# Kernel tuning notes

Measured on AMD Instinct MI355X. Metric: run time of the kernel, lower is better.

Reference implementation:

```python
import jax, jax.numpy as jnp
import numpy as np

N_NODES = 50000
N_EDGES = 800000
D = 64
N_GRAPHS = 512
N_LAYERS = 3
HID_FC = 64
N_CLASSES = 10


def setup_inputs() -> dict:
    key = jax.random.key(0)
    ks = jax.random.split(key, 12)
    s = 1.0 / np.sqrt(D)
    x = jax.random.normal(ks[0], (N_NODES, D), dtype=jnp.float32)
    edge_index = jax.random.randint(ks[1], (2, N_EDGES), 0, N_NODES, dtype=jnp.int32)
    batch = jnp.sort(jax.random.randint(ks[2], (N_NODES,), 0, N_GRAPHS, dtype=jnp.int32))
    convW1 = jax.random.normal(ks[3], (N_LAYERS, D, D), dtype=jnp.float32) * s
    convb1 = jax.random.normal(ks[4], (N_LAYERS, D), dtype=jnp.float32) * 0.01
    convW2 = jax.random.normal(ks[5], (N_LAYERS, D, D), dtype=jnp.float32) * s
    convb2 = jax.random.normal(ks[6], (N_LAYERS, D), dtype=jnp.float32) * 0.01
    fcW1 = jax.random.normal(ks[7], (D, HID_FC), dtype=jnp.float32) * s
    fcb1 = jax.random.normal(ks[8], (HID_FC,), dtype=jnp.float32) * 0.01
    fcW2 = jax.random.normal(ks[9], (HID_FC, N_CLASSES), dtype=jnp.float32) * (1.0 / np.sqrt(HID_FC))
    fcb2 = jax.random.normal(ks[10], (N_CLASSES,), dtype=jnp.float32) * 0.01
    return {"x": x, "convW1": convW1, "convb1": convb1, "convW2": convW2,
            "convb2": convb2, "fcW1": fcW1, "fcb1": fcb1, "fcW2": fcW2,
            "fcb2": fcb2, "edge_index": edge_index, "batch": batch}


def reference(x, convW1, convb1, convW2, convb2, fcW1, fcb1, fcW2, fcb2, edge_index, batch):
    src, dst = edge_index[0], edge_index[1]
    h = x
    for l in range(N_LAYERS):
        # GIN aggregation: (1 + eps) * x + sum_{j in N(i)} x_j, eps = 0
        agg = jax.ops.segment_sum(h[src], dst, num_segments=N_NODES)
        h = h + agg
        # per-layer MLP: Linear -> ReLU -> Linear
        h = jax.nn.relu(h @ convW1[l] + convb1[l])
        h = h @ convW2[l] + convb2[l]
    # global max pool over nodes of each graph
    g = jax.ops.segment_max(h, batch, num_segments=N_GRAPHS)
    # FC head: Linear(64) -> ReLU -> Linear(num_classes)
    g = jax.nn.relu(g @ fcW1 + fcb1)
    logits = g @ fcW2 + fcb2
    return jax.nn.log_softmax(logits, axis=1)
```

## Files before the change

### kernel.cpp

```cpp
#include <hip/hip_runtime.h>
#include <math.h>

#define N_NODES 50000
#define N_EDGES 800000
#define D 64
#define N_GRAPHS 512
#define N_CLASSES 10
#define NT 3125
#define NB32 1563
#define NPART 6250

#define SCAN_B 512
#define NB_SCAN ((N_NODES + SCAN_B - 1) / SCAN_B)

typedef __attribute__((ext_vector_type(8))) short bf16x8;
typedef __attribute__((ext_vector_type(4))) float f32x4;

#define MFMA16(a, b, c) __builtin_amdgcn_mfma_f32_16x16x32_bf16(a, b, c, 0, 0, 0)


__device__ __forceinline__ unsigned mapf(float f) {
  unsigned u = __float_as_uint(f);
  return (u & 0x80000000u) ? ~u : (u | 0x80000000u);
}
__device__ __forceinline__ float unmapf(unsigned u) {
  return __uint_as_float((u & 0x80000000u) ? (u & 0x7FFFFFFFu) : ~u);
}
__device__ __forceinline__ ushort bf16_rne(float f) {
  unsigned u = __float_as_uint(f);
  u += 0x7FFFu + ((u >> 16) & 1u);
  return (ushort)(u >> 16);
}
__device__ __forceinline__ float bf16_tof(ushort h) {
  return __uint_as_float(((unsigned)h) << 16);
}
__device__ __forceinline__ unsigned pack2(float a, float b) {
  return (unsigned)bf16_rne(a) | ((unsigned)bf16_rne(b) << 16);
}
__device__ __forceinline__ float2 unpack2(unsigned v) {
  return make_float2(__uint_as_float(v << 16), __uint_as_float(v & 0xFFFF0000u));
}


__global__ void wprep(const float* __restrict__ convW1, const float* __restrict__ convW2,
                      ushort* __restrict__ wf) {
  const int wi = blockIdx.x;
  const int layer = wi >> 1, which = wi & 1;
  const float* W = (which ? convW2 : convW1) + layer * 4096;
  const int t = threadIdx.x;
  const int f = t >> 6, lane = t & 63;
  const int ct = f >> 1, ks = f & 1;
  const int n = ct * 16 + (lane & 15);
  const int k0 = ks * 32 + ((lane >> 4) << 3);
  ushort hi[8], lo[8];
#pragma unroll
  for (int v = 0; v < 8; ++v) {
    float w = W[(k0 + v) * 64 + n];
    ushort h = bf16_rne(w);
    hi[v] = h;
    lo[v] = bf16_rne(w - bf16_tof(h));
  }
  ushort* base = wf + layer * 16384 + which * 8192;
  *(uint4*)(base + f * 512 + lane * 8) = *(uint4*)hi;
  *(uint4*)(base + 4096 + f * 512 + lane * 8) = *(uint4*)lo;
}


__global__ void hist_part(const int* __restrict__ dst, int* __restrict__ deg) {
  const int p = blockIdx.x & 7;
  const int lo = p * NPART, hi = lo + NPART;
  const int stride = (gridDim.x >> 3) * 256;
  for (int e = (blockIdx.x >> 3) * 256 + threadIdx.x; e < N_EDGES; e += stride) {
    int d = dst[e];
    if (d >= lo && d < hi) atomicAdd(&deg[d], 1);
  }
}

__global__ void scan_blocks(const int* __restrict__ deg, int* __restrict__ bsum) {
  __shared__ int sd[SCAN_B];
  int i = blockIdx.x * SCAN_B + threadIdx.x;
  sd[threadIdx.x] = (i < N_NODES) ? deg[i] : 0;
  __syncthreads();
  for (int off = SCAN_B / 2; off > 0; off >>= 1) {
    if (threadIdx.x < off) sd[threadIdx.x] += sd[threadIdx.x + off];
    __syncthreads();
  }
  if (threadIdx.x == 0) bsum[blockIdx.x] = sd[0];
}

__global__ void scan_mid(int* __restrict__ bsum) {
  __shared__ int s[256];
  int t = threadIdx.x;
  if (t < NB_SCAN) s[t] = bsum[t];
  __syncthreads();
  if (t == 0) {
    int run = 0;
    for (int i = 0; i < NB_SCAN; ++i) { int v = s[i]; s[i] = run; run += v; }
  }
  __syncthreads();
  if (t < NB_SCAN) bsum[t] = s[t];
}

__global__ void scan_final(const int* __restrict__ deg, const int* __restrict__ bsum,
                           int* __restrict__ rs, int* __restrict__ cur) {
  __shared__ int sd[SCAN_B];
  int i = blockIdx.x * SCAN_B + threadIdx.x;
  int v = (i < N_NODES) ? deg[i] : 0;
  sd[threadIdx.x] = v;
  __syncthreads();
  for (int off = 1; off < SCAN_B; off <<= 1) {
    int add = (threadIdx.x >= off) ? sd[threadIdx.x - off] : 0;
    __syncthreads();
    sd[threadIdx.x] += add;
    __syncthreads();
  }
  if (i < N_NODES) {
    int ex = bsum[blockIdx.x] + sd[threadIdx.x] - v;
    rs[i] = ex;
    cur[i] = ex;
  }
  if (i == 0) rs[N_NODES] = N_EDGES;
}

__global__ void fill_part(const int* __restrict__ src, const int* __restrict__ dst,
                          int* __restrict__ cur, int* __restrict__ csr) {
  const int p = blockIdx.x & 7;
  const int lo = p * NPART, hi = lo + NPART;
  const int stride = (gridDim.x >> 3) * 256;
  for (int e = (blockIdx.x >> 3) * 256 + threadIdx.x; e < N_EDGES; e += stride) {
    int d = dst[e];
    if (d >= lo && d < hi) {
      int pos = atomicAdd(&cur[d], 1);
      csr[pos] = src[e];
    }
  }
}


template <int FINAL, int F32IN>
__global__ __launch_bounds__(256, 4) void gin32(
    const void* __restrict__ hin_, unsigned* __restrict__ hout,
    const int* __restrict__ csr, const int* __restrict__ rs,
    const ushort* __restrict__ wfL,
    const float* __restrict__ b1, const float* __restrict__ b2,
    const int* __restrict__ batch, unsigned* __restrict__ gU) {
  __shared__ ushort Wl[16384];
  __shared__ ushort At[32][72];
  const int t = threadIdx.x;

  {
    const uint4* s = (const uint4*)wfL;
    uint4* d = (uint4*)Wl;
#pragma unroll
    for (int i = 0; i < 8; ++i) d[t + 256 * i] = s[t + 256 * i];
  }

  {
    const int qw = t >> 4, ql = t & 15;
    const float4* hf = (const float4*)hin_;
    const uint2* hb = (const uint2*)hin_;
#pragma unroll
    for (int i = 0; i < 2; ++i) {
      const int nl = qw + 16 * i;
      const int node = blockIdx.x * 32 + nl;
      float ax = 0.f, ay = 0.f, az = 0.f, aw = 0.f;
      if (node < N_NODES) {
        if (F32IN) {
          float4 v = hf[node * 16 + ql];
          ax = v.x; ay = v.y; az = v.z; aw = v.w;
        } else {
          uint2 u = hb[node * 16 + ql];
          float2 p0 = unpack2(u.x), p1 = unpack2(u.y);
          ax = p0.x; ay = p0.y; az = p1.x; aw = p1.y;
        }
        int e = rs[node];
        const int e1 = rs[node + 1];
        if (F32IN) {
          for (; e + 4 <= e1; e += 4) {
            int s0 = csr[e], s1 = csr[e + 1], s2 = csr[e + 2], s3 = csr[e + 3];
            float4 v0 = hf[s0 * 16 + ql];
            float4 v1 = hf[s1 * 16 + ql];
            float4 v2 = hf[s2 * 16 + ql];
            float4 v3 = hf[s3 * 16 + ql];
            ax += v0.x + v1.x; ay += v0.y + v1.y; az += v0.z + v1.z; aw += v0.w + v1.w;
            ax += v2.x + v3.x; ay += v2.y + v3.y; az += v2.z + v3.z; aw += v2.w + v3.w;
          }
          for (; e < e1; ++e) {
            float4 v = hf[csr[e] * 16 + ql];
            ax += v.x; ay += v.y; az += v.z; aw += v.w;
          }
        } else {
          for (; e + 4 <= e1; e += 4) {
            int s0 = csr[e], s1 = csr[e + 1], s2 = csr[e + 2], s3 = csr[e + 3];
            uint2 u0 = hb[s0 * 16 + ql];
            uint2 u1 = hb[s1 * 16 + ql];
            uint2 u2 = hb[s2 * 16 + ql];
            uint2 u3 = hb[s3 * 16 + ql];
            float2 q0, q1;
            q0 = unpack2(u0.x); q1 = unpack2(u0.y); ax += q0.x; ay += q0.y; az += q1.x; aw += q1.y;
            q0 = unpack2(u1.x); q1 = unpack2(u1.y); ax += q0.x; ay += q0.y; az += q1.x; aw += q1.y;
            q0 = unpack2(u2.x); q1 = unpack2(u2.y); ax += q0.x; ay += q0.y; az += q1.x; aw += q1.y;
            q0 = unpack2(u3.x); q1 = unpack2(u3.y); ax += q0.x; ay += q0.y; az += q1.x; aw += q1.y;
          }
          for (; e < e1; ++e) {
            uint2 u = hb[csr[e] * 16 + ql];
            float2 q0 = unpack2(u.x), q1 = unpack2(u.y);
            ax += q0.x; ay += q0.y; az += q1.x; aw += q1.y;
          }
        }
      }
      *(uint2*)&At[nl][4 * ql] = make_uint2(pack2(ax, ay), pack2(az, aw));
    }
  }
  __syncthreads();

  const int w = t >> 6, lane = t & 63;
  if (w >= 2) return;
  const int tile = blockIdx.x * 2 + w;
  if (tile >= NT) return;
  const int m = lane & 15, g = lane >> 4;
  ushort* tw = &At[w * 16][0];

  bf16x8 a0 = *(const bf16x8*)&At[w * 16 + m][g * 8];
  bf16x8 a1 = *(const bf16x8*)&At[w * 16 + m][32 + g * 8];
  const char* wb = (const char*)Wl + lane * 16;
#define LDW(off) (*(const bf16x8*)(wb + (off)))

  f32x4 c0 = {0.f, 0.f, 0.f, 0.f}, c1 = c0, c2 = c0, c3 = c0;
#define G1(ct, cc)                                      \
  cc = MFMA16(a0, LDW((2 * ct + 0) * 1024), cc);        \
  cc = MFMA16(a1, LDW((2 * ct + 1) * 1024), cc);        \
  cc = MFMA16(a0, LDW(8192 + (2 * ct + 0) * 1024), cc); \
  cc = MFMA16(a1, LDW(8192 + (2 * ct + 1) * 1024), cc);
  G1(0, c0) G1(1, c1) G1(2, c2) G1(3, c3)
#undef G1

  {
    float bv0 = b1[m], bv1 = b1[16 + m], bv2 = b1[32 + m], bv3 = b1[48 + m];
#define WRT(cc, ct, bv)                                                    \
    tw[(g * 4 + 0) * 72 + ct * 16 + m] = bf16_rne(fmaxf(cc[0] + bv, 0.f)); \
    tw[(g * 4 + 1) * 72 + ct * 16 + m] = bf16_rne(fmaxf(cc[1] + bv, 0.f)); \
    tw[(g * 4 + 2) * 72 + ct * 16 + m] = bf16_rne(fmaxf(cc[2] + bv, 0.f)); \
    tw[(g * 4 + 3) * 72 + ct * 16 + m] = bf16_rne(fmaxf(cc[3] + bv, 0.f));
    WRT(c0, 0, bv0) WRT(c1, 1, bv1) WRT(c2, 2, bv2) WRT(c3, 3, bv3)
#undef WRT
  }
  bf16x8 h0 = *(const bf16x8*)(tw + m * 72 + g * 8);
  bf16x8 h1 = *(const bf16x8*)(tw + m * 72 + 32 + g * 8);

  c0 = (f32x4){0.f, 0.f, 0.f, 0.f}; c1 = c0; c2 = c0; c3 = c0;
#define G2(ct, cc)                                       \
  cc = MFMA16(h0, LDW(16384 + (2 * ct + 0) * 1024), cc); \
  cc = MFMA16(h1, LDW(16384 + (2 * ct + 1) * 1024), cc); \
  cc = MFMA16(h0, LDW(24576 + (2 * ct + 0) * 1024), cc); \
  cc = MFMA16(h1, LDW(24576 + (2 * ct + 1) * 1024), cc);
  G2(0, c0) G2(1, c1) G2(2, c2) G2(3, c3)
#undef G2
#undef LDW

  const float bv20 = b2[m], bv21 = b2[16 + m], bv22 = b2[32 + m], bv23 = b2[48 + m];
  if (FINAL) {
    const int tb = tile * 16;
#define PM(cc, ct, bv, j)                                           \
    atomicMax(&gU[batch[tb + g * 4 + j] * 64 + ct * 16 + m], mapf(cc[j] + bv));
#define PM4(cc, ct, bv) PM(cc, ct, bv, 0) PM(cc, ct, bv, 1) PM(cc, ct, bv, 2) PM(cc, ct, bv, 3)
    PM4(c0, 0, bv20) PM4(c1, 1, bv21) PM4(c2, 2, bv22) PM4(c3, 3, bv23)
#undef PM4
#undef PM
  } else {
#define WRO(cc, ct, bv)                                        \
    tw[(g * 4 + 0) * 72 + ct * 16 + m] = bf16_rne(cc[0] + bv); \
    tw[(g * 4 + 1) * 72 + ct * 16 + m] = bf16_rne(cc[1] + bv); \
    tw[(g * 4 + 2) * 72 + ct * 16 + m] = bf16_rne(cc[2] + bv); \
    tw[(g * 4 + 3) * 72 + ct * 16 + m] = bf16_rne(cc[3] + bv);
    WRO(c0, 0, bv20) WRO(c1, 1, bv21) WRO(c2, 2, bv22) WRO(c3, 3, bv23)
#undef WRO
    const int r = lane >> 2, q = lane & 3;
    uint4 v0 = *(const uint4*)(tw + r * 72 + q * 16);
    uint4 v1 = *(const uint4*)(tw + r * 72 + q * 16 + 8);
    ushort* Ao = (ushort*)hout + (size_t)tile * 1024;
    *(uint4*)(Ao + lane * 16) = v0;
    *(uint4*)(Ao + lane * 16 + 8) = v1;
  }
}


__global__ void init_g(unsigned* __restrict__ gU) {
  int i = blockIdx.x * blockDim.x + threadIdx.x;
  if (i < N_GRAPHS * D) gU[i] = 0x007FFFFFu;
}

__global__ void head_kernel(const unsigned* __restrict__ gU,
                            const float* __restrict__ fcW1, const float* __restrict__ fcb1,
                            const float* __restrict__ fcW2, const float* __restrict__ fcb2,
                            float* __restrict__ out) {
  __shared__ float gbuf[64];
  __shared__ float hid[64];
  __shared__ float logit[N_CLASSES];
  __shared__ float red[2];
  const int gi = blockIdx.x;
  const int t = threadIdx.x;

  gbuf[t] = unmapf(gU[gi * D + t]);
  __syncthreads();

  float a = fcb1[t];
#pragma unroll
  for (int k = 0; k < 64; ++k) a = fmaf(gbuf[k], fcW1[k * 64 + t], a);
  hid[t] = fmaxf(a, 0.0f);
  __syncthreads();

  if (t < N_CLASSES) {
    float l = fcb2[t];
#pragma unroll
    for (int k = 0; k < 64; ++k) l = fmaf(hid[k], fcW2[k * N_CLASSES + t], l);
    logit[t] = l;
  }
  __syncthreads();

  if (t == 0) {
    float mx = logit[0];
    for (int i = 1; i < N_CLASSES; ++i) mx = fmaxf(mx, logit[i]);
    float s = 0.0f;
    for (int i = 0; i < N_CLASSES; ++i) s += expf(logit[i] - mx);
    red[0] = mx;
    red[1] = logf(s);
  }
  __syncthreads();

  if (t < N_CLASSES) out[gi * N_CLASSES + t] = logit[t] - red[0] - red[1];
}


extern "C" void kernel_launch(void* const* d_in, const int* in_sizes, int n_in,
                              void* d_out, int out_size, void* d_ws, size_t ws_size,
                              hipStream_t stream) {
  const float* x      = (const float*)d_in[0];
  const float* convW1 = (const float*)d_in[1];
  const float* convb1 = (const float*)d_in[2];
  const float* convW2 = (const float*)d_in[3];
  const float* convb2 = (const float*)d_in[4];
  const float* fcW1   = (const float*)d_in[5];
  const float* fcb1   = (const float*)d_in[6];
  const float* fcW2   = (const float*)d_in[7];
  const float* fcb2   = (const float*)d_in[8];
  const int*   edge   = (const int*)d_in[9];
  const int*   batch  = (const int*)d_in[10];
  float* out = (float*)d_out;

  const int* src = edge;
  const int* dst = edge + N_EDGES;

  unsigned* hbA = (unsigned*)d_ws;
  unsigned* hbB = hbA + (size_t)N_NODES * 32;
  unsigned* gU  = hbB + (size_t)N_NODES * 32;
  int* rs  = (int*)(gU + N_GRAPHS * D);
  int* csr = rs + N_NODES + 1;
  ushort* wf = (ushort*)(csr + N_EDGES);
  int* deg  = (int*)hbA;
  int* cur  = deg + N_NODES;
  int* bsum = cur + N_NODES;

  wprep<<<6, 512, 0, stream>>>(convW1, convW2, wf);
  init_g<<<(N_GRAPHS * D + 255) / 256, 256, 0, stream>>>(gU);

  hipMemsetAsync(deg, 0, N_NODES * sizeof(int), stream);
  hist_part<<<2048, 256, 0, stream>>>(dst, deg);
  scan_blocks<<<NB_SCAN, SCAN_B, 0, stream>>>(deg, bsum);
  scan_mid<<<1, 256, 0, stream>>>(bsum);
  scan_final<<<NB_SCAN, SCAN_B, 0, stream>>>(deg, bsum, rs, cur);
  fill_part<<<2048, 256, 0, stream>>>(src, dst, cur, csr);

  gin32<0, 1><<<NB32, 256, 0, stream>>>(x, hbA, csr, rs, wf,
                                        convb1, convb2, batch, gU);
  gin32<0, 0><<<NB32, 256, 0, stream>>>(hbA, hbB, csr, rs, wf + 16384,
                                        convb1 + 64, convb2 + 64, batch, gU);
  gin32<1, 0><<<NB32, 256, 0, stream>>>(hbB, nullptr, csr, rs, wf + 32768,
                                        convb1 + 128, convb2 + 128, batch, gU);

  head_kernel<<<N_GRAPHS, 64, 0, stream>>>(gU, fcW1, fcb1, fcW2, fcb2, out);
}
```

Before: 229.4 us.

## Fuse three GIN layer kernels into one persistent kernel with grid barriers

Replaces the three per-layer gin32 launches with a single persistent kernel of 1024 blocks that loops over node tiles and separates layers with a software grid barrier built on global atomics. The goal is to remove the launch gaps and tail drain between layers. In exchange, each block processes up to two tiles serially. The spin barrier depends on all 1024 blocks being co-resident, which the launch bounds (4 blocks per CU) should allow on 256 CUs.

```diff
diff --git a/kernel.cpp b/kernel.cpp
--- a/kernel.cpp
+++ b/kernel.cpp
@@ -9,6 +9,7 @@
 #define NT 3125
 #define NB32 1563
 #define NPART 6250
+#define MEGA_GRID 1024
 
 #define SCAN_B 512
 #define NB_SCAN ((N_NODES + SCAN_B - 1) / SCAN_B)
@@ -137,24 +138,42 @@
 }
 
 
-template <int FINAL, int F32IN>
-__global__ __launch_bounds__(256, 4) void gin32(
-    const void* __restrict__ hin_, unsigned* __restrict__ hout,
+__device__ __forceinline__ void stage_weights(const ushort* __restrict__ wfL,
+                                              ushort* Wl, int t) {
+  const uint4* s = (const uint4*)wfL;
+  uint4* d = (uint4*)Wl;
+#pragma unroll
+  for (int i = 0; i < 8; ++i) d[t + 256 * i] = s[t + 256 * i];
+}
+
+__device__ __forceinline__ void grid_barrier(unsigned* bar, int nb, int t) {
+  __threadfence();
+  __syncthreads();
+  if (t == 0) {
+    unsigned g = atomicAdd(&bar[1], 0u);
+    unsigned old = atomicAdd(&bar[0], 1u);
+    if (old == (unsigned)nb - 1u) {
+      atomicExch(&bar[0], 0u);
+      __threadfence();
+      atomicAdd(&bar[1], 1u);
+    } else {
+      unsigned spins = 0;
+      while (atomicAdd(&bar[1], 0u) == g) {
+        if (++spins > (1u << 30)) break;
+      }
+    }
+  }
+  __syncthreads();
+  __threadfence();
+}
+
+template <int F32IN, int FINAL>
+__device__ __forceinline__ void unit_body(
+    int unit, const void* __restrict__ hin_, unsigned* __restrict__ hout,
     const int* __restrict__ csr, const int* __restrict__ rs,
-    const ushort* __restrict__ wfL,
+    const ushort* Wl, ushort (*At)[72],
     const float* __restrict__ b1, const float* __restrict__ b2,
-    const int* __restrict__ batch, unsigned* __restrict__ gU) {
-  __shared__ ushort Wl[16384];
-  __shared__ ushort At[32][72];
-  const int t = threadIdx.x;
-
-  {
-    const uint4* s = (const uint4*)wfL;
-    uint4* d = (uint4*)Wl;
-#pragma unroll
-    for (int i = 0; i < 8; ++i) d[t + 256 * i] = s[t + 256 * i];
-  }
-
+    const int* __restrict__ batch, unsigned* __restrict__ gU, int t) {
   {
     const int qw = t >> 4, ql = t & 15;
     const float4* hf = (const float4*)hin_;
@@ -162,7 +181,7 @@
 #pragma unroll
     for (int i = 0; i < 2; ++i) {
       const int nl = qw + 16 * i;
-      const int node = blockIdx.x * 32 + nl;
+      const int node = unit * 32 + nl;
       float ax = 0.f, ay = 0.f, az = 0.f, aw = 0.f;
       if (node < N_NODES) {
         if (F32IN) {
@@ -215,73 +234,106 @@
   __syncthreads();
 
   const int w = t >> 6, lane = t & 63;
-  if (w >= 2) return;
-  const int tile = blockIdx.x * 2 + w;
-  if (tile >= NT) return;
-  const int m = lane & 15, g = lane >> 4;
-  ushort* tw = &At[w * 16][0];
-
-  bf16x8 a0 = *(const bf16x8*)&At[w * 16 + m][g * 8];
-  bf16x8 a1 = *(const bf16x8*)&At[w * 16 + m][32 + g * 8];
-  const char* wb = (const char*)Wl + lane * 16;
+  const int tile = unit * 2 + w;
+  if (w < 2 && tile < NT) {
+    const int m = lane & 15, g = lane >> 4;
+    ushort* tw = &At[w * 16][0];
+    bf16x8 a0 = *(const bf16x8*)&At[w * 16 + m][g * 8];
+    bf16x8 a1 = *(const bf16x8*)&At[w * 16 + m][32 + g * 8];
+    const char* wb = (const char*)Wl + lane * 16;
 #define LDW(off) (*(const bf16x8*)(wb + (off)))
 
-  f32x4 c0 = {0.f, 0.f, 0.f, 0.f}, c1 = c0, c2 = c0, c3 = c0;
+    f32x4 c0 = {0.f, 0.f, 0.f, 0.f}, c1 = c0, c2 = c0, c3 = c0;
 #define G1(ct, cc)                                      \
-  cc = MFMA16(a0, LDW((2 * ct + 0) * 1024), cc);        \
-  cc = MFMA16(a1, LDW((2 * ct + 1) * 1024), cc);        \
-  cc = MFMA16(a0, LDW(8192 + (2 * ct + 0) * 1024), cc); \
-  cc = MFMA16(a1, LDW(8192 + (2 * ct + 1) * 1024), cc);
-  G1(0, c0) G1(1, c1) G1(2, c2) G1(3, c3)
+    cc = MFMA16(a0, LDW((2 * ct + 0) * 1024), cc);      \
+    cc = MFMA16(a1, LDW((2 * ct + 1) * 1024), cc);      \
+    cc = MFMA16(a0, LDW(8192 + (2 * ct + 0) * 1024), cc); \
+    cc = MFMA16(a1, LDW(8192 + (2 * ct + 1) * 1024), cc);
+    G1(0, c0) G1(1, c1) G1(2, c2) G1(3, c3)
 #undef G1
 
-  {
-    float bv0 = b1[m], bv1 = b1[16 + m], bv2 = b1[32 + m], bv3 = b1[48 + m];
+    {
+      float bv0 = b1[m], bv1 = b1[16 + m], bv2 = b1[32 + m], bv3 = b1[48 + m];
 #define WRT(cc, ct, bv)                                                    \
-    tw[(g * 4 + 0) * 72 + ct * 16 + m] = bf16_rne(fmaxf(cc[0] + bv, 0.f)); \
-    tw[(g * 4 + 1) * 72 + ct * 16 + m] = bf16_rne(fmaxf(cc[1] + bv, 0.f)); \
-    tw[(g * 4 + 2) * 72 + ct * 16 + m] = bf16_rne(fmaxf(cc[2] + bv, 0.f)); \
-    tw[(g * 4 + 3) * 72 + ct * 16 + m] = bf16_rne(fmaxf(cc[3] + bv, 0.f));
-    WRT(c0, 0, bv0) WRT(c1, 1, bv1) WRT(c2, 2, bv2) WRT(c3, 3, bv3)
+      tw[(g * 4 + 0) * 72 + ct * 16 + m] = bf16_rne(fmaxf(cc[0] + bv, 0.f)); \
+      tw[(g * 4 + 1) * 72 + ct * 16 + m] = bf16_rne(fmaxf(cc[1] + bv, 0.f)); \
+      tw[(g * 4 + 2) * 72 + ct * 16 + m] = bf16_rne(fmaxf(cc[2] + bv, 0.f)); \
+      tw[(g * 4 + 3) * 72 + ct * 16 + m] = bf16_rne(fmaxf(cc[3] + bv, 0.f));
+      WRT(c0, 0, bv0) WRT(c1, 1, bv1) WRT(c2, 2, bv2) WRT(c3, 3, bv3)
 #undef WRT
-  }
-  bf16x8 h0 = *(const bf16x8*)(tw + m * 72 + g * 8);
-  bf16x8 h1 = *(const bf16x8*)(tw + m * 72 + 32 + g * 8);
-
-  c0 = (f32x4){0.f, 0.f, 0.f, 0.f}; c1 = c0; c2 = c0; c3 = c0;
+    }
+    bf16x8 h0 = *(const bf16x8*)(tw + m * 72 + g * 8);
+    bf16x8 h1 = *(const bf16x8*)(tw + m * 72 + 32 + g * 8);
+
+    c0 = (f32x4){0.f, 0.f, 0.f, 0.f}; c1 = c0; c2 = c0; c3 = c0;
 #define G2(ct, cc)                                       \
-  cc = MFMA16(h0, LDW(16384 + (2 * ct + 0) * 1024), cc); \
-  cc = MFMA16(h1, LDW(16384 + (2 * ct + 1) * 1024), cc); \
-  cc = MFMA16(h0, LDW(24576 + (2 * ct + 0) * 1024), cc); \
-  cc = MFMA16(h1, LDW(24576 + (2 * ct + 1) * 1024), cc);
-  G2(0, c0) G2(1, c1) G2(2, c2) G2(3, c3)
+    cc = MFMA16(h0, LDW(16384 + (2 * ct + 0) * 1024), cc); \
+    cc = MFMA16(h1, LDW(16384 + (2 * ct + 1) * 1024), cc); \
+    cc = MFMA16(h0, LDW(24576 + (2 * ct + 0) * 1024), cc); \
+    cc = MFMA16(h1, LDW(24576 + (2 * ct + 1) * 1024), cc);
+    G2(0, c0) G2(1, c1) G2(2, c2) G2(3, c3)
 #undef G2
 #undef LDW
 
-  const float bv20 = b2[m], bv21 = b2[16 + m], bv22 = b2[32 + m], bv23 = b2[48 + m];
-  if (FINAL) {
-    const int tb = tile * 16;
+    const float bv20 = b2[m], bv21 = b2[16 + m], bv22 = b2[32 + m], bv23 = b2[48 + m];
+    if (FINAL) {
+      const int tb = tile * 16;
 #define PM(cc, ct, bv, j)                                           \
-    atomicMax(&gU[batch[tb + g * 4 + j] * 64 + ct * 16 + m], mapf(cc[j] + bv));
+      atomicMax(&gU[batch[tb + g * 4 + j] * 64 + ct * 16 + m], mapf(cc[j] + bv));
 #define PM4(cc, ct, bv) PM(cc, ct, bv, 0) PM(cc, ct, bv, 1) PM(cc, ct, bv, 2) PM(cc, ct, bv, 3)
-    PM4(c0, 0, bv20) PM4(c1, 1, bv21) PM4(c2, 2, bv22) PM4(c3, 3, bv23)
+      PM4(c0, 0, bv20) PM4(c1, 1, bv21) PM4(c2, 2, bv22) PM4(c3, 3, bv23)
 #undef PM4
 #undef PM
-  } else {
+    } else {
 #define WRO(cc, ct, bv)                                        \
-    tw[(g * 4 + 0) * 72 + ct * 16 + m] = bf16_rne(cc[0] + bv); \
-    tw[(g * 4 + 1) * 72 + ct * 16 + m] = bf16_rne(cc[1] + bv); \
-    tw[(g * 4 + 2) * 72 + ct * 16 + m] = bf16_rne(cc[2] + bv); \
-    tw[(g * 4 + 3) * 72 + ct * 16 + m] = bf16_rne(cc[3] + bv);
-    WRO(c0, 0, bv20) WRO(c1, 1, bv21) WRO(c2, 2, bv22) WRO(c3, 3, bv23)
+      tw[(g * 4 + 0) * 72 + ct * 16 + m] = bf16_rne(cc[0] + bv); \
+      tw[(g * 4 + 1) * 72 + ct * 16 + m] = bf16_rne(cc[1] + bv); \
+      tw[(g * 4 + 2) * 72 + ct * 16 + m] = bf16_rne(cc[2] + bv); \
+      tw[(g * 4 + 3) * 72 + ct * 16 + m] = bf16_rne(cc[3] + bv);
+      WRO(c0, 0, bv20) WRO(c1, 1, bv21) WRO(c2, 2, bv22) WRO(c3, 3, bv23)
 #undef WRO
-    const int r = lane >> 2, q = lane & 3;
-    uint4 v0 = *(const uint4*)(tw + r * 72 + q * 16);
-    uint4 v1 = *(const uint4*)(tw + r * 72 + q * 16 + 8);
-    ushort* Ao = (ushort*)hout + (size_t)tile * 1024;
-    *(uint4*)(Ao + lane * 16) = v0;
-    *(uint4*)(Ao + lane * 16 + 8) = v1;
-  }
+      const int r = lane >> 2, q = lane & 3;
+      uint4 v0 = *(const uint4*)(tw + r * 72 + q * 16);
+      uint4 v1 = *(const uint4*)(tw + r * 72 + q * 16 + 8);
+      ushort* Ao = (ushort*)hout + (size_t)tile * 1024;
+      *(uint4*)(Ao + lane * 16) = v0;
+      *(uint4*)(Ao + lane * 16 + 8) = v1;
+    }
+  }
+  __syncthreads();
+}
+
+
+__global__ __launch_bounds__(256, 4) void gin_mega(
+    const float* __restrict__ x, unsigned* __restrict__ hbA, unsigned* __restrict__ hbB,
+    const int* __restrict__ csr, const int* __restrict__ rs,
+    const ushort* __restrict__ wf,
+    const float* __restrict__ convb1, const float* __restrict__ convb2,
+    const int* __restrict__ batch, unsigned* __restrict__ gU,
+    unsigned* __restrict__ bar) {
+  __shared__ ushort Wl[16384];
+  __shared__ ushort At[32][72];
+  const int t = threadIdx.x;
+  const int bid = blockIdx.x;
+
+  stage_weights(wf, Wl, t);
+  __syncthreads();
+  for (int u = bid; u < NB32; u += MEGA_GRID)
+    unit_body<1, 0>(u, x, hbA, csr, rs, Wl, At, convb1, convb2, batch, gU, t);
+  grid_barrier(bar, MEGA_GRID, t);
+
+  stage_weights(wf + 16384, Wl, t);
+  __syncthreads();
+  for (int u = bid; u < NB32; u += MEGA_GRID)
+    unit_body<0, 0>(u, hbA, hbB, csr, rs, Wl, At, convb1 + 64, convb2 + 64,
+                    batch, gU, t);
+  grid_barrier(bar + 2, MEGA_GRID, t);
+
+  stage_weights(wf + 32768, Wl, t);
+  __syncthreads();
+  for (int u = bid; u < NB32; u += MEGA_GRID)
+    unit_body<0, 1>(u, hbB, nullptr, csr, rs, Wl, At, convb1 + 128, convb2 + 128,
+                    batch, gU, t);
 }
 
 
@@ -357,12 +409,14 @@
   int* rs  = (int*)(gU + N_GRAPHS * D);
   int* csr = rs + N_NODES + 1;
   ushort* wf = (ushort*)(csr + N_EDGES);
+  unsigned* bar = (unsigned*)(wf + 49152);
   int* deg  = (int*)hbA;
   int* cur  = deg + N_NODES;
   int* bsum = cur + N_NODES;
 
   wprep<<<6, 512, 0, stream>>>(convW1, convW2, wf);
   init_g<<<(N_GRAPHS * D + 255) / 256, 256, 0, stream>>>(gU);
+  hipMemsetAsync(bar, 0, 4 * sizeof(unsigned), stream);
 
   hipMemsetAsync(deg, 0, N_NODES * sizeof(int), stream);
   hist_part<<<2048, 256, 0, stream>>>(dst, deg);
@@ -371,12 +425,8 @@
   scan_final<<<NB_SCAN, SCAN_B, 0, stream>>>(deg, bsum, rs, cur);
   fill_part<<<2048, 256, 0, stream>>>(src, dst, cur, csr);
 
-  gin32<0, 1><<<NB32, 256, 0, stream>>>(x, hbA, csr, rs, wf,
-                                        convb1, convb2, batch, gU);
-  gin32<0, 0><<<NB32, 256, 0, stream>>>(hbA, hbB, csr, rs, wf + 16384,
-                                        convb1 + 64, convb2 + 64, batch, gU);
-  gin32<1, 0><<<NB32, 256, 0, stream>>>(hbB, nullptr, csr, rs, wf + 32768,
-                                        convb1 + 128, convb2 + 128, batch, gU);
+  gin_mega<<<MEGA_GRID, 256, 0, stream>>>(x, hbA, hbB, csr, rs, wf,
+                                          convb1, convb2, batch, gU, bar);
 
   head_kernel<<<N_GRAPHS, 64, 0, stream>>>(gU, fcW1, fcb1, fcW2, fcb2, out);
 }
```

New measurement: 712.3 us. +210.5%, slower.
